# Kernel optimization log

Hardware: AMD Instinct MI355X
Metric: run time of the kernel (lower is better)

Reference implementation:

```python
import jax, jax.numpy as jnp
import numpy as np

D_MODEL = 1024
NUM_ATOMS = 16384
TEMPERATURE = 1.0
NEG_INF = -1e9


def setup_inputs() -> dict:
    key = jax.random.key(0)
    kx, kd, km = jax.random.split(key, 3)
    x = jax.random.normal(kx, (4, 2048, D_MODEL), dtype=jnp.float32)
    # xavier_uniform for [num_atoms, d_model]
    limit = float(np.sqrt(6.0 / (NUM_ATOMS + D_MODEL)))
    dictionary = jax.random.uniform(
        kd, (NUM_ATOMS, D_MODEL), dtype=jnp.float32, minval=-limit, maxval=limit
    )
    mask = jax.random.randint(km, (4, 2048, NUM_ATOMS), 0, 2, dtype=jnp.int32)
    return {"x": x, "dictionary": dictionary, "mask": mask}


def reference(x, dictionary, mask):
    # scores: [b, s, num_atoms]
    scores = jnp.einsum("bsd,ad->bsa", x, dictionary)
    m = mask.astype(scores.dtype)
    scores = scores * m + (1.0 - m) * NEG_INF
    weights = jax.nn.softmax(scores / TEMPERATURE, axis=-1)
    reconstruction = jnp.einsum("bsa,ad->bsd", weights, dictionary)
    argmax_indices = jnp.argmax(scores, axis=-1)
    return reconstruction, argmax_indices
```

## Files before the change

### kernel.cpp

```cpp
#include <hip/hip_runtime.h>

#define NTOK   8192
#define DMODEL 1024
#define NATOM  16384

typedef _Float16 half8  __attribute__((ext_vector_type(8)));
typedef _Float16 half4_t __attribute__((ext_vector_type(4)));
typedef float    f32x4  __attribute__((ext_vector_type(4)));

#define GLOAD_LDS16(gsrc, ldst) \
  __builtin_amdgcn_global_load_lds((const __attribute__((address_space(1))) unsigned int*)(gsrc), \
                                   (__attribute__((address_space(3))) unsigned int*)(ldst), 16, 0, 0)

__global__ void cvt_f32_f16(const float* __restrict__ in, _Float16* __restrict__ out, int n4) {
  int i = blockIdx.x * 256 + threadIdx.x;
  if (i >= n4) return;
  float4 v = ((const float4*)in)[i];
  half4_t h;
  h[0] = (_Float16)v.x; h[1] = (_Float16)v.y; h[2] = (_Float16)v.z; h[3] = (_Float16)v.w;
  ((half4_t*)out)[i] = h;
}

__global__ void transpose_dict(const float* __restrict__ dict, _Float16* __restrict__ dT) {
  __shared__ _Float16 tile[64][68];
  int a0 = blockIdx.x * 64;
  int d0 = blockIdx.y * 64;
  int tid = threadIdx.x;
  int c = tid & 63;
  int r0 = tid >> 6;
  #pragma unroll
  for (int i = 0; i < 16; i++) {
    int r = r0 + i * 4;
    tile[r][c] = (_Float16)dict[(size_t)(a0 + r) * DMODEL + d0 + c];
  }
  __syncthreads();
  #pragma unroll
  for (int i = 0; i < 16; i++) {
    int rd = r0 + i * 4;
    dT[(size_t)(d0 + rd) * NATOM + a0 + c] = tile[c][rd];
  }
}

__launch_bounds__(256, 2)
__global__ void score_kernel(const _Float16* __restrict__ Xh,
                             const _Float16* __restrict__ Dh,
                             const int* __restrict__ mask,
                             _Float16* __restrict__ E) {
  __shared__ _Float16 lds[17408];
  _Float16* As = lds;
  _Float16* Bs = lds + 4096;
  const int tid  = threadIdx.x;
  const int lane = tid & 63;
  const int wave = tid >> 6;
  const int wm = wave >> 1, wn = wave & 1;
  const int m0 = blockIdx.y * 128;
  const int n0 = blockIdx.x * 128;

  const int frow = lane & 15;
  const int fkc  = lane >> 4;

  f32x4 acc[4][4] = {};

  for (int k0 = 0; k0 < DMODEL; k0 += 32) {
    __syncthreads();
    #pragma unroll
    for (int i = 0; i < 2; i++) {
      int L = tid + i * 256;
      int r = L >> 2, pc = L & 3;
      int c = pc ^ ((r >> 1) & 3);
      GLOAD_LDS16(Xh + (size_t)(m0 + r) * DMODEL + k0 + c * 8, As + (size_t)L * 8);
      GLOAD_LDS16(Dh + (size_t)(n0 + r) * DMODEL + k0 + c * 8, Bs + (size_t)L * 8);
    }
    __syncthreads();
    half8 af[4], bf[4];
    #pragma unroll
    for (int i = 0; i < 4; i++) {
      int ar = wm * 64 + i * 16 + frow;
      int br = wn * 64 + i * 16 + frow;
      af[i] = *(const half8*)&As[ar * 32 + (fkc ^ ((ar >> 1) & 3)) * 8];
      bf[i] = *(const half8*)&Bs[br * 32 + (fkc ^ ((br >> 1) & 3)) * 8];
    }
    #pragma unroll
    for (int i = 0; i < 4; i++)
      #pragma unroll
      for (int j = 0; j < 4; j++)
        acc[i][j] = __builtin_amdgcn_mfma_f32_16x16x32_f16(af[i], bf[j], acc[i][j], 0, 0, 0);
  }

  __syncthreads();
  const int cr = (lane >> 4) * 4;
  const int cc = lane & 15;
  #pragma unroll
  for (int i = 0; i < 4; i++) {
    #pragma unroll
    for (int j = 0; j < 4; j++) {
      #pragma unroll
      for (int r = 0; r < 4; r++) {
        int lr = wm * 64 + i * 16 + cr + r;
        int lc = wn * 64 + j * 16 + cc;
        int mk = mask[(size_t)(m0 + lr) * NATOM + (n0 + lc)];
        float e = mk ? __expf(acc[i][j][r]) : 0.0f;
        lds[lr * 136 + lc] = (_Float16)e;
      }
    }
  }
  __syncthreads();
  #pragma unroll
  for (int i = 0; i < 8; i++) {
    int chunk = i * 256 + tid;
    int r  = chunk >> 4;
    int c8 = (chunk & 15) * 8;
    *(half8*)&E[(size_t)(m0 + r) * NATOM + n0 + c8] = *(const half8*)&lds[r * 136 + c8];
  }
}

__global__ void scan_kernel(const _Float16* __restrict__ E,
                            const float* __restrict__ x,
                            const float* __restrict__ dict,
                            float* __restrict__ lsum,
                            float* __restrict__ argout) {
  const int t = blockIdx.x;
  const int tid = threadIdx.x;
  const int lane = tid & 63;
  const int wid = tid >> 6;
  const _Float16* row = E + (size_t)t * NATOM;

  half8 v[8];
  float mx = 0.0f, sm = 0.0f;
  #pragma unroll
  for (int i = 0; i < 8; i++) {
    v[i] = *(const half8*)&row[i * 2048 + tid * 8];
    #pragma unroll
    for (int j = 0; j < 8; j++) {
      float f = (float)v[i][j];
      sm += f;
      mx = fmaxf(mx, f);
    }
  }
  #pragma unroll
  for (int off = 32; off > 0; off >>= 1) {
    mx = fmaxf(mx, __shfl_down(mx, off, 64));
    sm += __shfl_down(sm, off, 64);
  }
  __shared__ float wmx[4], wsm[4];
  __shared__ float bmax, bsum;
  __shared__ int cnt;
  __shared__ int cand[64];
  __shared__ double csc[64];
  __shared__ double dred[4];
  if (lane == 0) { wmx[wid] = mx; wsm[wid] = sm; }
  if (tid == 0) cnt = 0;
  __syncthreads();
  if (tid == 0) {
    bmax = fmaxf(fmaxf(wmx[0], wmx[1]), fmaxf(wmx[2], wmx[3]));
    bsum = wsm[0] + wsm[1] + wsm[2] + wsm[3];
  }
  __syncthreads();
  float thr = bmax * 0.98f;
  if (bmax > 0.0f) {
    #pragma unroll
    for (int i = 0; i < 8; i++) {
      #pragma unroll
      for (int j = 0; j < 8; j++) {
        if ((float)v[i][j] >= thr) {
          int p = atomicAdd(&cnt, 1);
          if (p < 64) cand[p] = i * 2048 + tid * 8 + j;
        }
      }
    }
  }
  __syncthreads();
  int nc = min(cnt, 64);
  for (int c = 0; c < nc; c++) {
    const float* dr = dict + (size_t)cand[c] * DMODEL;
    const float* xr = x + (size_t)t * DMODEL;
    double a = 0.0;
    for (int d = tid; d < DMODEL; d += 256)
      a += (double)xr[d] * (double)dr[d];
    #pragma unroll
    for (int off = 32; off > 0; off >>= 1)
      a += __shfl_down(a, off, 64);
    if (lane == 0) dred[wid] = a;
    __syncthreads();
    if (tid == 0) csc[c] = dred[0] + dred[1] + dred[2] + dred[3];
    __syncthreads();
  }
  if (tid == 0) {
    lsum[t] = bsum;
    int best = 0;
    if (nc > 0) {
      double bs = -1e300;
      best = NATOM;
      for (int c = 0; c < nc; c++) {
        if (csc[c] > bs || (csc[c] == bs && cand[c] < best)) { bs = csc[c]; best = cand[c]; }
      }
    }
    argout[t] = (float)best;
  }
}

__launch_bounds__(256, 2)
__global__ void recon_kernel(const _Float16* __restrict__ E,
                             const _Float16* __restrict__ DT,
                             const float* __restrict__ lsum,
                             float* __restrict__ out) {
  __shared__ _Float16 lds[10240];
  _Float16* As = lds;
  _Float16* Bs = lds + 2048;
  const int tid  = threadIdx.x;
  const int lane = tid & 63;
  const int wave = tid >> 6;
  const int m0 = blockIdx.y * 64;
  const int n0 = blockIdx.x * 256;

  const int frow = lane & 15;
  const int fkc  = lane >> 4;

  f32x4 acc[4][4] = {};

  for (int k0 = 0; k0 < NATOM; k0 += 32) {
    __syncthreads();
    {
      int L = tid;
      int r = L >> 2, pc = L & 3;
      int c = pc ^ ((r >> 1) & 3);
      GLOAD_LDS16(E + (size_t)(m0 + r) * NATOM + k0 + c * 8, As + (size_t)L * 8);
    }
    #pragma unroll
    for (int i = 0; i < 4; i++) {
      int L = tid + i * 256;
      int r = L >> 2, pc = L & 3;
      int c = pc ^ ((r >> 1) & 3);
      GLOAD_LDS16(DT + (size_t)(n0 + r) * NATOM + k0 + c * 8, Bs + (size_t)L * 8);
    }
    __syncthreads();
    half8 af[4], bf[4];
    #pragma unroll
    for (int i = 0; i < 4; i++) {
      int ar = i * 16 + frow;
      int br = wave * 64 + i * 16 + frow;
      af[i] = *(const half8*)&As[ar * 32 + (fkc ^ ((ar >> 1) & 3)) * 8];
      bf[i] = *(const half8*)&Bs[br * 32 + (fkc ^ ((br >> 1) & 3)) * 8];
    }
    #pragma unroll
    for (int i = 0; i < 4; i++)
      #pragma unroll
      for (int j = 0; j < 4; j++)
        acc[i][j] = __builtin_amdgcn_mfma_f32_16x16x32_f16(af[i], bf[j], acc[i][j], 0, 0, 0);
  }

  const int cr = (lane >> 4) * 4;
  const int cc = lane & 15;
  #pragma unroll
  for (int i = 0; i < 4; i++) {
    #pragma unroll
    for (int r = 0; r < 4; r++) {
      int lr = i * 16 + cr + r;
      float sc = 1.0f / lsum[m0 + lr];
      #pragma unroll
      for (int j = 0; j < 4; j++) {
        int lc = wave * 64 + j * 16 + cc;
        out[(size_t)(m0 + lr) * DMODEL + (n0 + lc)] = acc[i][j][r] * sc;
      }
    }
  }
}

extern "C" void kernel_launch(void* const* d_in, const int* in_sizes, int n_in,
                              void* d_out, int out_size, void* d_ws, size_t ws_size,
                              hipStream_t stream) {
  const float* x    = (const float*)d_in[0];
  const float* dict = (const float*)d_in[1];
  const int*   mask = (const int*)d_in[2];
  float* recon  = (float*)d_out;
  float* argout = recon + (size_t)NTOK * DMODEL;

  char* w = (char*)d_ws;
  _Float16* Xh = (_Float16*)(w);
  _Float16* Dh = (_Float16*)(w + (size_t)16  * 1024 * 1024);
  _Float16* DT = (_Float16*)(w + (size_t)48  * 1024 * 1024);
  _Float16* E  = (_Float16*)(w + (size_t)80  * 1024 * 1024);
  float*  lsum = (float*)  (w + (size_t)336 * 1024 * 1024);

  cvt_f32_f16<<<dim3(NTOK * DMODEL / 4 / 256), 256, 0, stream>>>(x, Xh, NTOK * DMODEL / 4);
  cvt_f32_f16<<<dim3(NATOM * DMODEL / 4 / 256), 256, 0, stream>>>(dict, Dh, NATOM * DMODEL / 4);
  transpose_dict<<<dim3(NATOM / 64, DMODEL / 64), 256, 0, stream>>>(dict, DT);
  score_kernel<<<dim3(NATOM / 128, NTOK / 128), 256, 0, stream>>>(Xh, Dh, mask, E);
  scan_kernel<<<dim3(NTOK), 256, 0, stream>>>(E, x, dict, lsum, argout);
  recon_kernel<<<dim3(DMODEL / 256, NTOK / 64), 256, 0, stream>>>(E, DT, lsum, recon);
}
```

Measured before the change: 1.656 ms.

## Fuse row sums/max into score epilogue, double-buffer GEMMs, lighten argmax scan

Score kernel now accumulates per-row exp sums via atomics and writes per-tile maxima, so the scan kernel no longer rereads the full E matrix. It only revisits tiles whose max is near the row max to pick argmax candidates. Both GEMM kernels get double-buffered LDS staging to overlap global loads with MFMA. The dictionary f16 conversion is merged into the transpose kernel, which removes one launch and one read of the dictionary. This adds atomics and uses the output buffer as temporary scratch for the tile maxima.

```diff
diff --git a/kernel.cpp b/kernel.cpp
--- a/kernel.cpp
+++ b/kernel.cpp
@@ -21,7 +21,8 @@
   ((half4_t*)out)[i] = h;
 }
 
-__global__ void transpose_dict(const float* __restrict__ dict, _Float16* __restrict__ dT) {
+__global__ void transpose_dict(const float* __restrict__ dict,
+                               _Float16* __restrict__ Dh, _Float16* __restrict__ dT) {
   __shared__ _Float16 tile[64][68];
   int a0 = blockIdx.x * 64;
   int d0 = blockIdx.y * 64;
@@ -31,13 +32,34 @@
   #pragma unroll
   for (int i = 0; i < 16; i++) {
     int r = r0 + i * 4;
-    tile[r][c] = (_Float16)dict[(size_t)(a0 + r) * DMODEL + d0 + c];
+    _Float16 h = (_Float16)dict[(size_t)(a0 + r) * DMODEL + d0 + c];
+    tile[r][c] = h;
+    Dh[(size_t)(a0 + r) * DMODEL + d0 + c] = h;
   }
   __syncthreads();
   #pragma unroll
   for (int i = 0; i < 16; i++) {
     int rd = r0 + i * 4;
     dT[(size_t)(d0 + rd) * NATOM + a0 + c] = tile[c][rd];
+  }
+}
+
+__global__ void zero_lsum(float* __restrict__ lsum) {
+  lsum[blockIdx.x * 256 + threadIdx.x] = 0.0f;
+}
+
+__device__ __forceinline__ void stage_ab(const _Float16* __restrict__ A,
+                                         const _Float16* __restrict__ B,
+                                         _Float16* As, _Float16* Bs,
+                                         size_t arow0, size_t brow0, size_t ldk,
+                                         int k0, int tid) {
+  #pragma unroll
+  for (int i = 0; i < 2; i++) {
+    int L = tid + i * 256;
+    int r = L >> 2, pc = L & 3;
+    int c = pc ^ ((r >> 1) & 3);
+    GLOAD_LDS16(A + (arow0 + r) * ldk + k0 + c * 8, As + (size_t)L * 8);
+    GLOAD_LDS16(B + (brow0 + r) * ldk + k0 + c * 8, Bs + (size_t)L * 8);
   }
 }
 
@@ -45,10 +67,10 @@
 __global__ void score_kernel(const _Float16* __restrict__ Xh,
                              const _Float16* __restrict__ Dh,
                              const int* __restrict__ mask,
-                             _Float16* __restrict__ E) {
+                             _Float16* __restrict__ E,
+                             float* __restrict__ lsum,
+                             _Float16* __restrict__ Tmax) {
   __shared__ _Float16 lds[17408];
-  _Float16* As = lds;
-  _Float16* Bs = lds + 4096;
   const int tid  = threadIdx.x;
   const int lane = tid & 63;
   const int wave = tid >> 6;
@@ -61,17 +83,15 @@
 
   f32x4 acc[4][4] = {};
 
-  for (int k0 = 0; k0 < DMODEL; k0 += 32) {
+  stage_ab(Xh, Dh, lds, lds + 4096, m0, n0, DMODEL, 0, tid);
+  int cur = 0;
+  for (int it = 0; it < DMODEL / 32; ++it) {
     __syncthreads();
-    #pragma unroll
-    for (int i = 0; i < 2; i++) {
-      int L = tid + i * 256;
-      int r = L >> 2, pc = L & 3;
-      int c = pc ^ ((r >> 1) & 3);
-      GLOAD_LDS16(Xh + (size_t)(m0 + r) * DMODEL + k0 + c * 8, As + (size_t)L * 8);
-      GLOAD_LDS16(Dh + (size_t)(n0 + r) * DMODEL + k0 + c * 8, Bs + (size_t)L * 8);
-    }
-    __syncthreads();
+    if (it + 1 < DMODEL / 32)
+      stage_ab(Xh, Dh, lds + (cur ^ 1) * 8192, lds + (cur ^ 1) * 8192 + 4096,
+               m0, n0, DMODEL, (it + 1) * 32, tid);
+    _Float16* As = lds + cur * 8192;
+    _Float16* Bs = As + 4096;
     half8 af[4], bf[4];
     #pragma unroll
     for (int i = 0; i < 4; i++) {
@@ -85,6 +105,7 @@
       #pragma unroll
       for (int j = 0; j < 4; j++)
         acc[i][j] = __builtin_amdgcn_mfma_f32_16x16x32_f16(af[i], bf[j], acc[i][j], 0, 0, 0);
+    cur ^= 1;
   }
 
   __syncthreads();
@@ -112,88 +133,81 @@
     int c8 = (chunk & 15) * 8;
     *(half8*)&E[(size_t)(m0 + r) * NATOM + n0 + c8] = *(const half8*)&lds[r * 136 + c8];
   }
-}
-
-__global__ void scan_kernel(const _Float16* __restrict__ E,
-                            const float* __restrict__ x,
-                            const float* __restrict__ dict,
-                            float* __restrict__ lsum,
-                            float* __restrict__ argout) {
+  {
+    int r = tid >> 1, h = tid & 1;
+    const _Float16* rowp = &lds[r * 136 + h * 64];
+    float s = 0.0f, m = 0.0f;
+    #pragma unroll
+    for (int i = 0; i < 8; i++) {
+      half8 v = *(const half8*)&rowp[i * 8];
+      #pragma unroll
+      for (int j = 0; j < 8; j++) { float f = (float)v[j]; s += f; m = fmaxf(m, f); }
+    }
+    s += __shfl_xor(s, 1, 64);
+    m = fmaxf(m, __shfl_xor(m, 1, 64));
+    if (h == 0) {
+      atomicAdd(&lsum[m0 + r], s);
+      Tmax[(size_t)blockIdx.x * NTOK + m0 + r] = (_Float16)m;
+    }
+  }
+}
+
+__global__ void scan_lite(const _Float16* __restrict__ E,
+                          const _Float16* __restrict__ Tmax,
+                          const float* __restrict__ x,
+                          const float* __restrict__ dict,
+                          float* __restrict__ argout) {
   const int t = blockIdx.x;
-  const int tid = threadIdx.x;
-  const int lane = tid & 63;
-  const int wid = tid >> 6;
-  const _Float16* row = E + (size_t)t * NATOM;
-
-  half8 v[8];
-  float mx = 0.0f, sm = 0.0f;
-  #pragma unroll
-  for (int i = 0; i < 8; i++) {
-    v[i] = *(const half8*)&row[i * 2048 + tid * 8];
-    #pragma unroll
-    for (int j = 0; j < 8; j++) {
-      float f = (float)v[i][j];
-      sm += f;
-      mx = fmaxf(mx, f);
-    }
-  }
-  #pragma unroll
-  for (int off = 32; off > 0; off >>= 1) {
-    mx = fmaxf(mx, __shfl_down(mx, off, 64));
-    sm += __shfl_down(sm, off, 64);
-  }
-  __shared__ float wmx[4], wsm[4];
-  __shared__ float bmax, bsum;
+  const int lane = threadIdx.x;
+  float m0 = (float)Tmax[(size_t)lane * NTOK + t];
+  float m1 = (float)Tmax[(size_t)(64 + lane) * NTOK + t];
+  float mx = fmaxf(m0, m1);
+  #pragma unroll
+  for (int off = 32; off > 0; off >>= 1) mx = fmaxf(mx, __shfl_xor(mx, off, 64));
+
   __shared__ int cnt;
-  __shared__ int cand[64];
-  __shared__ double csc[64];
-  __shared__ double dred[4];
-  if (lane == 0) { wmx[wid] = mx; wsm[wid] = sm; }
-  if (tid == 0) cnt = 0;
-  __syncthreads();
-  if (tid == 0) {
-    bmax = fmaxf(fmaxf(wmx[0], wmx[1]), fmaxf(wmx[2], wmx[3]));
-    bsum = wsm[0] + wsm[1] + wsm[2] + wsm[3];
-  }
-  __syncthreads();
-  float thr = bmax * 0.98f;
-  if (bmax > 0.0f) {
-    #pragma unroll
-    for (int i = 0; i < 8; i++) {
-      #pragma unroll
-      for (int j = 0; j < 8; j++) {
-        if ((float)v[i][j] >= thr) {
-          int p = atomicAdd(&cnt, 1);
-          if (p < 64) cand[p] = i * 2048 + tid * 8 + j;
-        }
-      }
-    }
-  }
-  __syncthreads();
-  int nc = min(cnt, 64);
+  __shared__ int cand[32];
+  __shared__ double csc[32];
+  if (lane == 0) cnt = 0;
+  __syncthreads();
+
+  if (mx > 0.0f) {
+    float thr = 0.98f * mx;
+    unsigned long long q0 = __ballot(m0 >= thr);
+    unsigned long long q1 = __ballot(m1 >= thr);
+    while (q0 | q1) {
+      int tile;
+      if (q0) { tile = __ffsll(q0) - 1; q0 &= q0 - 1; }
+      else    { tile = 64 + __ffsll(q1) - 1; q1 &= q1 - 1; }
+      const _Float16* ep = E + (size_t)t * NATOM + tile * 128;
+      float e0 = (float)ep[lane], e1 = (float)ep[64 + lane];
+      if (e0 >= thr) { int p = atomicAdd(&cnt, 1); if (p < 32) cand[p] = tile * 128 + lane; }
+      if (e1 >= thr) { int p = atomicAdd(&cnt, 1); if (p < 32) cand[p] = tile * 128 + 64 + lane; }
+    }
+  }
+  __syncthreads();
+  int nc = min(cnt, 32);
+  const float* xr = x + (size_t)t * DMODEL;
   for (int c = 0; c < nc; c++) {
     const float* dr = dict + (size_t)cand[c] * DMODEL;
-    const float* xr = x + (size_t)t * DMODEL;
     double a = 0.0;
-    for (int d = tid; d < DMODEL; d += 256)
+    #pragma unroll
+    for (int i = 0; i < 16; i++) {
+      int d = lane + i * 64;
       a += (double)xr[d] * (double)dr[d];
-    #pragma unroll
-    for (int off = 32; off > 0; off >>= 1)
-      a += __shfl_down(a, off, 64);
-    if (lane == 0) dred[wid] = a;
-    __syncthreads();
-    if (tid == 0) csc[c] = dred[0] + dred[1] + dred[2] + dred[3];
-    __syncthreads();
-  }
-  if (tid == 0) {
-    lsum[t] = bsum;
+    }
+    #pragma unroll
+    for (int off = 32; off > 0; off >>= 1) a += __shfl_down(a, off, 64);
+    if (lane == 0) csc[c] = a;
+  }
+  __syncthreads();
+  if (lane == 0) {
     int best = 0;
     if (nc > 0) {
       double bs = -1e300;
       best = NATOM;
-      for (int c = 0; c < nc; c++) {
+      for (int c = 0; c < nc; c++)
         if (csc[c] > bs || (csc[c] == bs && cand[c] < best)) { bs = csc[c]; best = cand[c]; }
-      }
     }
     argout[t] = (float)best;
   }
@@ -204,9 +218,7 @@
                              const _Float16* __restrict__ DT,
                              const float* __restrict__ lsum,
                              float* __restrict__ out) {
-  __shared__ _Float16 lds[10240];
-  _Float16* As = lds;
-  _Float16* Bs = lds + 2048;
+  __shared__ _Float16 lds[20480];
   const int tid  = threadIdx.x;
   const int lane = tid & 63;
   const int wave = tid >> 6;
@@ -218,8 +230,9 @@
 
   f32x4 acc[4][4] = {};
 
-  for (int k0 = 0; k0 < NATOM; k0 += 32) {
-    __syncthreads();
+  auto stage = [&](int k0, int b) {
+    _Float16* As = lds + b * 10240;
+    _Float16* Bs = As + 2048;
     {
       int L = tid;
       int r = L >> 2, pc = L & 3;
@@ -233,7 +246,15 @@
       int c = pc ^ ((r >> 1) & 3);
       GLOAD_LDS16(DT + (size_t)(n0 + r) * NATOM + k0 + c * 8, Bs + (size_t)L * 8);
     }
+  };
+
+  stage(0, 0);
+  int cur = 0;
+  for (int it = 0; it < NATOM / 32; ++it) {
     __syncthreads();
+    if (it + 1 < NATOM / 32) stage((it + 1) * 32, cur ^ 1);
+    _Float16* As = lds + cur * 10240;
+    _Float16* Bs = As + 2048;
     half8 af[4], bf[4];
     #pragma unroll
     for (int i = 0; i < 4; i++) {
@@ -247,6 +268,7 @@
       #pragma unroll
       for (int j = 0; j < 4; j++)
         acc[i][j] = __builtin_amdgcn_mfma_f32_16x16x32_f16(af[i], bf[j], acc[i][j], 0, 0, 0);
+    cur ^= 1;
   }
 
   const int cr = (lane >> 4) * 4;
@@ -281,11 +303,12 @@
   _Float16* DT = (_Float16*)(w + (size_t)48  * 1024 * 1024);
   _Float16* E  = (_Float16*)(w + (size_t)80  * 1024 * 1024);
   float*  lsum = (float*)  (w + (size_t)336 * 1024 * 1024);
+  _Float16* Tmax = (_Float16*)d_out;
 
   cvt_f32_f16<<<dim3(NTOK * DMODEL / 4 / 256), 256, 0, stream>>>(x, Xh, NTOK * DMODEL / 4);
-  cvt_f32_f16<<<dim3(NATOM * DMODEL / 4 / 256), 256, 0, stream>>>(dict, Dh, NATOM * DMODEL / 4);
-  transpose_dict<<<dim3(NATOM / 64, DMODEL / 64), 256, 0, stream>>>(dict, DT);
-  score_kernel<<<dim3(NATOM / 128, NTOK / 128), 256, 0, stream>>>(Xh, Dh, mask, E);
-  scan_kernel<<<dim3(NTOK), 256, 0, stream>>>(E, x, dict, lsum, argout);
+  transpose_dict<<<dim3(NATOM / 64, DMODEL / 64), 256, 0, stream>>>(dict, Dh, DT);
+  zero_lsum<<<dim3(NTOK / 256), 256, 0, stream>>>(lsum);
+  score_kernel<<<dim3(NATOM / 128, NTOK / 128), 256, 0, stream>>>(Xh, Dh, mask, E, lsum, Tmax);
+  scan_lite<<<dim3(NTOK), 64, 0, stream>>>(E, Tmax, x, dict, argout);
   recon_kernel<<<dim3(DMODEL / 256, NTOK / 64), 256, 0, stream>>>(E, DT, lsum, recon);
 }
```

Measured after the change: 1.494 ms. -9.8%, faster.
